# Optimization experiments

Measured on AMD Instinct MI355X. Metric: run time of the kernel, lower is better.

Reference implementation:

```python
import jax, jax.numpy as jnp
import numpy as np

D_MODEL = 1024
D_HEAD = 64
MAX_REL = 8
B, T = 4, 4096


def setup_inputs() -> dict:
    key = jax.random.key(0)
    k1, k2, k3, k4, k5 = jax.random.split(key, 5)
    return {
        "x": jax.random.normal(k1, (B, T, D_MODEL), dtype=jnp.float32),
        "W_q": jax.random.normal(k2, (D_HEAD, D_MODEL), dtype=jnp.float32) * (1.0 / np.sqrt(D_MODEL)),
        "W_k": jax.random.normal(k3, (D_HEAD, D_MODEL), dtype=jnp.float32) * (1.0 / np.sqrt(D_MODEL)),
        "W_v": jax.random.normal(k4, (D_HEAD, D_MODEL), dtype=jnp.float32) * (1.0 / np.sqrt(D_MODEL)),
        "rel_emb": jax.random.normal(k5, (2 * MAX_REL + 1, 1), dtype=jnp.float32),
    }


def reference(x, W_q, W_k, W_v, rel_emb):
    Bb, Tt, _ = x.shape
    scale = jnp.sqrt(jnp.asarray(W_q.shape[0], dtype=x.dtype))
    # projections (Linear: x @ W.T)
    q = jnp.einsum("btd,hd->bth", x, W_q)
    k = jnp.einsum("btd,hd->bth", x, W_k)
    v = jnp.einsum("btd,hd->bth", x, W_v)
    scores = jnp.einsum("bth,bsh->bts", q, k) / scale  # [B,T,T]
    # relative position bias: rel_emb[clip(j-i, -M, M) + M]
    i_idx = jnp.arange(Tt)[:, None]
    j_idx = jnp.arange(Tt)[None, :]
    rel = jnp.clip(j_idx - i_idx, -MAX_REL, MAX_REL) + MAX_REL  # [T,T] int
    rel_bias = rel_emb[rel, 0]  # [T,T]
    scores = scores + rel_bias[None, :, :]
    causal = j_idx <= i_idx  # [T,T] lower-triangular
    scores = jnp.where(causal[None, :, :], scores, -jnp.inf)
    attn = jax.nn.softmax(scores, axis=-1)
    return jnp.einsum("bts,bsh->bth", attn, v)
```

## Files before the change

kernel.cpp:

```cpp
#include <hip/hip_runtime.h>
#include <hip/hip_bf16.h>

#define BT 4
#define TT 4096
#define DM 1024
#define DH 64
#define NRE 17
#define LOG2E 1.4426950408889634f

using bf16 = __hip_bfloat16;
typedef __attribute__((ext_vector_type(8))) short short8;
typedef __attribute__((ext_vector_type(4))) short short4v;
typedef __attribute__((ext_vector_type(4))) float float4v;

static __device__ __forceinline__ short8 load8(const bf16* p) {
    return *reinterpret_cast<const short8*>(p);
}
static __device__ __forceinline__ short bfbits(float x) {
    return (short)__bfloat16_as_ushort(__float2bfloat16(x));
}
static __device__ __forceinline__ short8 pack8(float4v a, float4v b) {
    short8 r;
    r[0] = bfbits(a[0]); r[1] = bfbits(a[1]); r[2] = bfbits(a[2]); r[3] = bfbits(a[3]);
    r[4] = bfbits(b[0]); r[5] = bfbits(b[1]); r[6] = bfbits(b[2]); r[7] = bfbits(b[3]);
    return r;
}
static __device__ __forceinline__ void gload_lds16(const void* g, void* l) {
    __builtin_amdgcn_global_load_lds(
        (const __attribute__((address_space(1))) void*)g,
        (__attribute__((address_space(3))) void*)l, 16, 0, 0);
}


__global__ __launch_bounds__(256) void w_prep(
    const float* __restrict__ Wq, const float* __restrict__ Wk,
    const float* __restrict__ Wv, bf16* __restrict__ Wswz)
{
    const unsigned g = blockIdx.x * 256 + threadIdx.x;
    const unsigned c    = g / 768;
    const unsigned rem  = g - c * 768;
    const unsigned pair = rem >> 3;
    const unsigned slot = rem & 7;
    const unsigned l    = slot ^ (pair & 7);
    const unsigned row  = 2 * pair + (l >> 2);
    const unsigned k    = 32 * c + (l & 3) * 8;
    const float* src = (row < 64) ? &Wq[(size_t)row * DM + k]
                     : (row < 128) ? &Wk[(size_t)(row - 64) * DM + k]
                                   : &Wv[(size_t)(row - 128) * DM + k];
    float4v a = *reinterpret_cast<const float4v*>(src);
    float4v b = *reinterpret_cast<const float4v*>(src + 4);
    *reinterpret_cast<short8*>(&Wswz[(size_t)g * 8]) = pack8(a, b);
}

__global__ __launch_bounds__(256, 2) void qkv_gemm(
    const float* __restrict__ x, const bf16* __restrict__ Wswz,
    bf16* __restrict__ Qb, bf16* __restrict__ Kswz, bf16* __restrict__ Vswz)
{
    __shared__ float xs[2][64 * 32];
    __shared__ short Wls[2][96 * 64];
    __shared__ short Kimg[4096];
    __shared__ short Vimg[4096];

    const int w    = threadIdx.x >> 6;
    const int lane = threadIdx.x & 63;
    const int quad = lane >> 4;
    const int l16  = lane & 15;
    const int row0 = blockIdx.x * 64;
    const int b_   = row0 >> 12;
    const int tile = (row0 & (TT - 1)) >> 6;

    float4v acc[12];
#pragma unroll
    for (int i = 0; i < 12; i++) acc[i] = (float4v)(0.f);

    auto stage = [&](int c, int p) {
#pragma unroll
        for (int i = 0; i < 2; i++) {
            const int call = 2 * w + i;
            const int row  = call * 8 + (lane >> 3);
            const int ul   = (lane & 7) ^ (row & 7);
            gload_lds16(&x[(size_t)(row0 + row) * DM + c * 32 + ul * 4],
                        &xs[p][call * 256]);
        }
#pragma unroll
        for (int i = 0; i < 3; i++) {
            const int call = 3 * w + i;
            gload_lds16(&Wswz[(size_t)c * 6144 + call * 512 + lane * 8],
                        &Wls[p][call * 512]);
        }
    };

    stage(0, 0);

    for (int c = 0; c < 32; c++) {
        const int p = c & 1;
        __syncthreads();
        if (c + 1 < 32) stage(c + 1, p ^ 1);

        const int R = 16 * w + l16;
        float4v a0 = *reinterpret_cast<const float4v*>(
            &xs[p][R * 32 + 4 * ((2 * quad) ^ (l16 & 7))]);
        float4v a1 = *reinterpret_cast<const float4v*>(
            &xs[p][R * 32 + 4 * ((2 * quad + 1) ^ (l16 & 7))]);
        short8 a = pack8(a0, a1);
#pragma unroll
        for (int nt = 0; nt < 12; nt++) {
            const int pair = 8 * nt + (l16 >> 1);
            const int phys = ((l16 & 1) * 4 + quad) ^ (l16 >> 1);
            short8 bfr = *reinterpret_cast<const short8*>(&Wls[p][pair * 64 + phys * 8]);
            acc[nt] = __builtin_amdgcn_mfma_f32_16x16x32_bf16(a, bfr, acc[nt], 0, 0, 0);
        }
    }

#pragma unroll
    for (int nt = 0; nt < 12; nt++) {
#pragma unroll
        for (int r = 0; r < 4; r++) {
            const short hb = bfbits(acc[nt][r]);
            if (nt < 4) {
                const int i = row0 + 16 * w + quad * 4 + r;
                Qb[(size_t)i * DH + 16 * nt + l16] = __hip_bfloat16_raw{(unsigned short)hb};
            } else if (nt < 8) {
                const int h  = (nt - 4) >> 1;
                const int qk = ((nt - 4) & 1) * 2 + (l16 >> 3);
                Kimg[((2 * w + h) * 64 + qk * 16 + 4 * quad + r) * 8 + (l16 & 7)] = hb;
            }
        }
        if (nt >= 8) {
            const int dh = (nt - 8) >> 1;
            const int h8 = (nt - 8) & 1;
            short4v sv;
#pragma unroll
            for (int r = 0; r < 4; r++) sv[r] = bfbits(acc[nt][r]);
            *reinterpret_cast<short4v*>(
                &Vimg[((2 * w + dh) * 64 + quad * 16 + l16) * 8 + h8 * 4]) = sv;
        }
    }
    __syncthreads();
    {
        const size_t base = ((size_t)b_ * 64 + tile) * 4096;
#pragma unroll
        for (int i = 0; i < 2; i++) {
            const int u = threadIdx.x + 256 * i;
            *reinterpret_cast<short8*>(&Kswz[base + (size_t)u * 8]) =
                *reinterpret_cast<const short8*>(&Kimg[u * 8]);
            *reinterpret_cast<short8*>(&Vswz[base + (size_t)u * 8]) =
                *reinterpret_cast<const short8*>(&Vimg[u * 8]);
        }
    }
}

__global__ __launch_bounds__(256, 2) void attn(
    const bf16* __restrict__ Qb, const bf16* __restrict__ Kswz,
    const bf16* __restrict__ Vswz, const float* __restrict__ rel,
    float* __restrict__ out)
{
    __shared__ short sbuf[2][16384];

    const int w     = threadIdx.x >> 6;
    const int lane  = threadIdx.x & 63;
    const int quad  = lane >> 4;
    const int l16   = lane & 15;
    const int qh    = w & 1;
    const int strm  = w >> 1;
    const int batch = blockIdx.x & 3;
    const int u     = blockIdx.x >> 2;
    const int t     = (u < 64) ? u : (191 - u);
    const int q0    = 32 * t;

    const float SCL = 0.125f * LOG2E;
    const float relreg = (lane < NRE) ? rel[lane] * LOG2E : 0.f;
    const float rel0 = __shfl(relreg, 0, 64);

    const size_t bbase = (size_t)batch * TT;
    const int i_row = q0 + 16 * qh + l16;

    short8 bq0, bq1;
    {
        const bf16* qp = &Qb[(bbase + i_row) * DH];
        bq0 = load8(qp + quad * 8);
        bq1 = load8(qp + 32 + quad * 8);
    }

    float4v o[4];
#pragma unroll
    for (int dt = 0; dt < 4; dt++) o[dt] = (float4v)(0.f);
    float m_st = -1e30f, l_st = 0.f;

    const int J = (q0 + 32 + 63) >> 6;
    const int C = (J + 1) >> 1;

    auto stage = [&](int c1, int p) {
        const int T = 2 * c1 + (w & 1);
        if (T >= J) return;
        const bf16* g = ((w < 2) ? Kswz : Vswz) + ((size_t)(batch * 64 + T)) * 4096;
#pragma unroll
        for (int call = 0; call < 8; call++)
            gload_lds16(g + call * 512 + lane * 8, &sbuf[p][w * 4096 + call * 512]);
    };

    stage(0, 0);

    for (int c = 0; c < C; c++) {
        const int p = c & 1;
        __syncthreads();
        if (c + 1 < C) stage(c + 1, p ^ 1);

        const int T = 2 * c + strm;
        if (T < J) {
            const int js = 64 * T;
            const short* Kl = &sbuf[p][strm * 4096];
            const short* Vl = &sbuf[p][8192 + strm * 4096];

            float4v st[4];
#pragma unroll
            for (int nt = 0; nt < 4; nt++) st[nt] = (float4v)(0.f);
#pragma unroll
            for (int nt = 0; nt < 4; nt++) {
                short8 k0 = *reinterpret_cast<const short8*>(Kl + (2 * nt) * 512 + lane * 8);
                short8 k1 = *reinterpret_cast<const short8*>(Kl + (2 * nt + 1) * 512 + lane * 8);
                st[nt] = __builtin_amdgcn_mfma_f32_16x16x32_bf16(k0, bq0, st[nt], 0, 0, 0);
                st[nt] = __builtin_amdgcn_mfma_f32_16x16x32_bf16(k1, bq1, st[nt], 0, 0, 0);
            }

            float mcur = -1e30f;
            if (js + 71 <= q0 + 16 * qh) {
#pragma unroll
                for (int nt = 0; nt < 4; nt++)
#pragma unroll
                    for (int r = 0; r < 4; r++) {
                        float v = st[nt][r] * SCL + rel0;
                        st[nt][r] = v;
                        mcur = fmaxf(mcur, v);
                    }
            } else {
#pragma unroll
                for (int nt = 0; nt < 4; nt++) {
                    const int jb = js + 16 * nt + 4 * quad;
#pragma unroll
                    for (int r = 0; r < 4; r++) {
                        const int d = jb + r - i_row;
                        int idx = d + 8;
                        idx = idx < 0 ? 0 : (idx > 16 ? 16 : idx);
                        float v = st[nt][r] * SCL + __shfl(relreg, idx, 64);
                        v = (d > 0) ? -1e30f : v;
                        st[nt][r] = v;
                        mcur = fmaxf(mcur, v);
                    }
                }
            }

            mcur = fmaxf(mcur, __shfl_xor(mcur, 16, 64));
            mcur = fmaxf(mcur, __shfl_xor(mcur, 32, 64));

            const float mn = fmaxf(m_st, mcur);
            const float alpha = exp2f(m_st - mn);
            m_st = mn;

            float lsum = 0.f;
            short4v pb[4];
#pragma unroll
            for (int nt = 0; nt < 4; nt++)
#pragma unroll
                for (int r = 0; r < 4; r++) {
                    const float e = exp2f(st[nt][r] - mn);
                    lsum += e;
                    pb[nt][r] = bfbits(e);
                }
            lsum += __shfl_xor(lsum, 16, 64);
            lsum += __shfl_xor(lsum, 32, 64);
            l_st = l_st * alpha + lsum;

#pragma unroll
            for (int dt = 0; dt < 4; dt++)
#pragma unroll
                for (int r = 0; r < 4; r++) o[dt][r] *= alpha;

#pragma unroll
            for (int nt = 0; nt < 4; nt++) {
#pragma unroll
                for (int dh = 0; dh < 2; dh++) {
                    short8 vs = *reinterpret_cast<const short8*>(
                        Vl + (nt * 2 + dh) * 512 + lane * 8);
                    short4v lo, hi;
                    lo[0] = vs[0]; lo[1] = vs[1]; lo[2] = vs[2]; lo[3] = vs[3];
                    hi[0] = vs[4]; hi[1] = vs[5]; hi[2] = vs[6]; hi[3] = vs[7];
                    o[2 * dh]     = __builtin_amdgcn_mfma_f32_16x16x16bf16_1k(lo, pb[nt], o[2 * dh], 0, 0, 0);
                    o[2 * dh + 1] = __builtin_amdgcn_mfma_f32_16x16x16bf16_1k(hi, pb[nt], o[2 * dh + 1], 0, 0, 0);
                }
            }
        }
    }

    __syncthreads();
    float* Osh = (float*)&sbuf[0][0];
    float* mM  = Osh + 4 * 16 * 68;
    float* lL  = mM + 64;

    const int slot = (strm * 2 + qh) * 16 + l16;
    if (quad == 0) { mM[slot] = m_st; lL[slot] = l_st; }
#pragma unroll
    for (int dt = 0; dt < 4; dt++)
        *reinterpret_cast<float4v*>(
            &Osh[((strm * 2 + qh) * 16 + l16) * 68 + 16 * dt + 4 * quad]) = o[dt];
    __syncthreads();

    for (int idx = threadIdx.x; idx < 32 * 64; idx += 256) {
        const int row = idx >> 6;
        const int qh2 = row >> 4, lr = row & 15;
        const int c2  = idx & 63;
        const float m0 = mM[(0 * 2 + qh2) * 16 + lr];
        const float m1 = mM[(1 * 2 + qh2) * 16 + lr];
        const float M = fmaxf(m0, m1);
        const float e0 = exp2f(m0 - M), e1 = exp2f(m1 - M);
        const float L = lL[(0 * 2 + qh2) * 16 + lr] * e0 + lL[(1 * 2 + qh2) * 16 + lr] * e1;
        const float acc = Osh[((0 * 2 + qh2) * 16 + lr) * 68 + c2] * e0
                        + Osh[((1 * 2 + qh2) * 16 + lr) * 68 + c2] * e1;
        out[(bbase + q0 + row) * DH + c2] = acc / L;
    }
}

extern "C" void kernel_launch(void* const* d_in, const int* in_sizes, int n_in,
                              void* d_out, int out_size, void* d_ws, size_t ws_size,
                              hipStream_t stream)
{
    const float* x   = (const float*)d_in[0];
    const float* Wq  = (const float*)d_in[1];
    const float* Wk  = (const float*)d_in[2];
    const float* Wv  = (const float*)d_in[3];
    const float* rel = (const float*)d_in[4];
    float* out = (float*)d_out;

    bf16* Qb   = (bf16*)d_ws;
    bf16* Kswz = Qb   + (size_t)BT * TT * DH;
    bf16* Vswz = Kswz + (size_t)BT * TT * DH;
    bf16* Wswz = Vswz + (size_t)BT * TT * DH;

    w_prep<<<96, 256, 0, stream>>>(Wq, Wk, Wv, Wswz);
    qkv_gemm<<<256, 256, 0, stream>>>(x, Wswz, Qb, Kswz, Vswz);
    attn<<<512, 256, 0, stream>>>(Qb, Kswz, Vswz, rel, out);
}
```

Baseline: 170.7 us.

## Restructure QKV GEMM and attention into 32-row tiles with per-wave KV streams

The QKV GEMM now uses 32-row blocks (twice as many blocks) with a 64-wide K step, splits the output columns across waves, and reads LDS through inline ds_read_b128 with a single wait. K/V are re-laid out as 32-key tiles. Attention is reorganised so each of four waves owns its own stream of 32-key tiles, double-buffered per wave without block-wide barriers, handling both 16-row query halves, and a 4-way merge combines the partial softmax states. The block-to-query-tile mapping is also changed. The goals are more parallelism, finer causal granularity and less barrier stalling, at the cost of more merge work and more register pressure.

```diff
diff --git a/kernel.cpp b/kernel.cpp
--- a/kernel.cpp
+++ b/kernel.cpp
@@ -13,6 +13,8 @@
 typedef __attribute__((ext_vector_type(4))) short short4v;
 typedef __attribute__((ext_vector_type(4))) float float4v;
 
+#define BC8(x) __builtin_bit_cast(short8, x)
+
 static __device__ __forceinline__ short8 load8(const bf16* p) {
     return *reinterpret_cast<const short8*>(p);
 }
@@ -30,6 +32,12 @@
         (const __attribute__((address_space(1))) void*)g,
         (__attribute__((address_space(3))) void*)l, 16, 0, 0);
 }
+static __device__ __forceinline__ unsigned lds_addr(const void* p) {
+    return (unsigned)(size_t)(const __attribute__((address_space(3))) void*)p;
+}
+
+#define DSR(dst, addr, off) \
+    asm volatile("ds_read_b128 %0, %1 offset:" off : "=v"(dst) : "v"(addr))
 
 
 __global__ __launch_bounds__(256) void w_prep(
@@ -56,97 +64,123 @@
     const float* __restrict__ x, const bf16* __restrict__ Wswz,
     bf16* __restrict__ Qb, bf16* __restrict__ Kswz, bf16* __restrict__ Vswz)
 {
-    __shared__ float xs[2][64 * 32];
-    __shared__ short Wls[2][96 * 64];
-    __shared__ short Kimg[4096];
-    __shared__ short Vimg[4096];
+    __shared__ __align__(16) float xs[2][2048];
+    __shared__ __align__(16) short Wls[2][12288];
 
     const int w    = threadIdx.x >> 6;
     const int lane = threadIdx.x & 63;
     const int quad = lane >> 4;
     const int l16  = lane & 15;
-    const int row0 = blockIdx.x * 64;
-    const int b_   = row0 >> 12;
-    const int tile = (row0 & (TT - 1)) >> 6;
-
-    float4v acc[12];
-#pragma unroll
-    for (int i = 0; i < 12; i++) acc[i] = (float4v)(0.f);
+    const int half = w & 1;
+    const int colh = w >> 1;
+    const int row0 = blockIdx.x * 32;
+
+    float4v acc[6];
+#pragma unroll
+    for (int i = 0; i < 6; i++) acc[i] = (float4v)(0.f);
 
     auto stage = [&](int c, int p) {
 #pragma unroll
-        for (int i = 0; i < 2; i++) {
-            const int call = 2 * w + i;
-            const int row  = call * 8 + (lane >> 3);
-            const int ul   = (lane & 7) ^ (row & 7);
-            gload_lds16(&x[(size_t)(row0 + row) * DM + c * 32 + ul * 4],
+        for (int j = 0; j < 2; j++) {
+            const int call = 2 * w + j;
+            const int row  = 4 * call + (lane >> 4);
+            const int pu   = lane & 15;
+            const int gu   = (pu & 8) | ((pu ^ row) & 7);
+            gload_lds16(&x[(size_t)(row0 + row) * DM + c * 64 + gu * 4],
                         &xs[p][call * 256]);
         }
 #pragma unroll
-        for (int i = 0; i < 3; i++) {
-            const int call = 3 * w + i;
-            gload_lds16(&Wswz[(size_t)c * 6144 + call * 512 + lane * 8],
+        for (int j = 0; j < 6; j++) {
+            const int call = 6 * w + j;
+            gload_lds16(&Wswz[(size_t)(2 * c) * 6144 + call * 512 + lane * 8],
                         &Wls[p][call * 512]);
         }
     };
 
+    const unsigned xlds = lds_addr(&xs[0][0]);
+    const unsigned wlds = lds_addr(&Wls[0][0]);
+    const int R        = 16 * half + l16;
+    const int lo3_0    = (2 * quad)     ^ (R & 7);
+    const int lo3_1    = (2 * quad + 1) ^ (R & 7);
+    const int pairBase = 48 * colh + (l16 >> 1);
+    const int physW    = ((l16 & 1) * 4 + quad) ^ ((l16 >> 1) & 7);
+
     stage(0, 0);
 
-    for (int c = 0; c < 32; c++) {
+    for (int c = 0; c < 16; c++) {
         const int p = c & 1;
         __syncthreads();
-        if (c + 1 < 32) stage(c + 1, p ^ 1);
-
-        const int R = 16 * w + l16;
-        float4v a0 = *reinterpret_cast<const float4v*>(
-            &xs[p][R * 32 + 4 * ((2 * quad) ^ (l16 & 7))]);
-        float4v a1 = *reinterpret_cast<const float4v*>(
-            &xs[p][R * 32 + 4 * ((2 * quad + 1) ^ (l16 & 7))]);
-        short8 a = pack8(a0, a1);
-#pragma unroll
-        for (int nt = 0; nt < 12; nt++) {
-            const int pair = 8 * nt + (l16 >> 1);
-            const int phys = ((l16 & 1) * 4 + quad) ^ (l16 >> 1);
-            short8 bfr = *reinterpret_cast<const short8*>(&Wls[p][pair * 64 + phys * 8]);
-            acc[nt] = __builtin_amdgcn_mfma_f32_16x16x32_bf16(a, bfr, acc[nt], 0, 0, 0);
-        }
-    }
-
-#pragma unroll
-    for (int nt = 0; nt < 12; nt++) {
+        if (c + 1 < 16) stage(c + 1, p ^ 1);
+
+        const unsigned xb  = xlds + (unsigned)(p * 8192) + R * 64 * 4;
+        const unsigned xa0 = xb + lo3_0 * 16;
+        const unsigned xa1 = xb + lo3_1 * 16;
+        const unsigned wa  = wlds + (unsigned)(p * 24576) + pairBase * 128 + physW * 16;
+
+        float4v x00, x01, x10, x11;
+        float4v w00, w01, w02, w03, w04, w05, w10, w11, w12, w13, w14, w15;
+        DSR(x00, xa0, "0");   DSR(x10, xa0, "128");
+        DSR(x01, xa1, "0");   DSR(x11, xa1, "128");
+        DSR(w00, wa, "0");     DSR(w01, wa, "1024");  DSR(w02, wa, "2048");
+        DSR(w03, wa, "3072");  DSR(w04, wa, "4096");  DSR(w05, wa, "5120");
+        DSR(w10, wa, "12288"); DSR(w11, wa, "13312"); DSR(w12, wa, "14336");
+        DSR(w13, wa, "15360"); DSR(w14, wa, "16384"); DSR(w15, wa, "17408");
+        asm volatile("s_waitcnt lgkmcnt(0)"
+            : "+v"(x00), "+v"(x01), "+v"(x10), "+v"(x11),
+              "+v"(w00), "+v"(w01), "+v"(w02), "+v"(w03), "+v"(w04), "+v"(w05),
+              "+v"(w10), "+v"(w11), "+v"(w12), "+v"(w13), "+v"(w14), "+v"(w15));
+
+        short8 a0 = pack8(x00, x01);
+        short8 a1 = pack8(x10, x11);
+        acc[0] = __builtin_amdgcn_mfma_f32_16x16x32_bf16(a0, BC8(w00), acc[0], 0, 0, 0);
+        acc[1] = __builtin_amdgcn_mfma_f32_16x16x32_bf16(a0, BC8(w01), acc[1], 0, 0, 0);
+        acc[2] = __builtin_amdgcn_mfma_f32_16x16x32_bf16(a0, BC8(w02), acc[2], 0, 0, 0);
+        acc[3] = __builtin_amdgcn_mfma_f32_16x16x32_bf16(a0, BC8(w03), acc[3], 0, 0, 0);
+        acc[4] = __builtin_amdgcn_mfma_f32_16x16x32_bf16(a0, BC8(w04), acc[4], 0, 0, 0);
+        acc[5] = __builtin_amdgcn_mfma_f32_16x16x32_bf16(a0, BC8(w05), acc[5], 0, 0, 0);
+        acc[0] = __builtin_amdgcn_mfma_f32_16x16x32_bf16(a1, BC8(w10), acc[0], 0, 0, 0);
+        acc[1] = __builtin_amdgcn_mfma_f32_16x16x32_bf16(a1, BC8(w11), acc[1], 0, 0, 0);
+        acc[2] = __builtin_amdgcn_mfma_f32_16x16x32_bf16(a1, BC8(w12), acc[2], 0, 0, 0);
+        acc[3] = __builtin_amdgcn_mfma_f32_16x16x32_bf16(a1, BC8(w13), acc[3], 0, 0, 0);
+        acc[4] = __builtin_amdgcn_mfma_f32_16x16x32_bf16(a1, BC8(w14), acc[4], 0, 0, 0);
+        acc[5] = __builtin_amdgcn_mfma_f32_16x16x32_bf16(a1, BC8(w15), acc[5], 0, 0, 0);
+    }
+
+    __syncthreads();
+    short* Kimg = (short*)&xs[0][0];
+    short* Vimg = Kimg + 2048;
+#pragma unroll
+    for (int nt = 0; nt < 6; nt++) {
+        const int cc = 96 * colh + 16 * nt + l16;
 #pragma unroll
         for (int r = 0; r < 4; r++) {
+            const int jl = 16 * half + 4 * quad + r;
             const short hb = bfbits(acc[nt][r]);
-            if (nt < 4) {
-                const int i = row0 + 16 * w + quad * 4 + r;
-                Qb[(size_t)i * DH + 16 * nt + l16] = __hip_bfloat16_raw{(unsigned short)hb};
-            } else if (nt < 8) {
-                const int h  = (nt - 4) >> 1;
-                const int qk = ((nt - 4) & 1) * 2 + (l16 >> 3);
-                Kimg[((2 * w + h) * 64 + qk * 16 + 4 * quad + r) * 8 + (l16 & 7)] = hb;
+            if (cc < 64) {
+                Qb[(size_t)(row0 + jl) * DH + cc] = __hip_bfloat16_raw{(unsigned short)hb};
+            } else if (cc < 128) {
+                const int k  = cc - 64;
+                const int h  = k >> 5;
+                const int q2 = (k & 31) >> 3;
+                Kimg[((2 * half + h) * 64 + q2 * 16 + 4 * quad + r) * 8 + (k & 7)] = hb;
+            } else {
+                const int d  = cc - 128;
+                const int dh = d >> 5;
+                const int hi = (d >> 4) & 1;
+                Vimg[((2 * half + dh) * 64 + quad * 16 + (d & 15)) * 8 + hi * 4 + r] = hb;
             }
-        }
-        if (nt >= 8) {
-            const int dh = (nt - 8) >> 1;
-            const int h8 = (nt - 8) & 1;
-            short4v sv;
-#pragma unroll
-            for (int r = 0; r < 4; r++) sv[r] = bfbits(acc[nt][r]);
-            *reinterpret_cast<short4v*>(
-                &Vimg[((2 * w + dh) * 64 + quad * 16 + l16) * 8 + h8 * 4]) = sv;
         }
     }
     __syncthreads();
     {
-        const size_t base = ((size_t)b_ * 64 + tile) * 4096;
-#pragma unroll
-        for (int i = 0; i < 2; i++) {
-            const int u = threadIdx.x + 256 * i;
-            *reinterpret_cast<short8*>(&Kswz[base + (size_t)u * 8]) =
-                *reinterpret_cast<const short8*>(&Kimg[u * 8]);
-            *reinterpret_cast<short8*>(&Vswz[base + (size_t)u * 8]) =
-                *reinterpret_cast<const short8*>(&Vimg[u * 8]);
-        }
+        const int b_     = row0 >> 12;
+        const int tile32 = (row0 & (TT - 1)) >> 5;
+        const size_t base = ((size_t)(b_ * 512 + tile32 * 4)) * 512;
+        const int u = threadIdx.x;
+        *reinterpret_cast<short8*>(&Kswz[base + (size_t)u * 8]) =
+            *reinterpret_cast<const short8*>(&Kimg[u * 8]);
+        *reinterpret_cast<short8*>(&Vswz[base + (size_t)u * 8]) =
+            *reinterpret_cast<const short8*>(&Vimg[u * 8]);
     }
 }
 
@@ -155,96 +189,110 @@
     const bf16* __restrict__ Vswz, const float* __restrict__ rel,
     float* __restrict__ out)
 {
-    __shared__ short sbuf[2][16384];
+    __shared__ __align__(16) short sbuf[32768];
 
     const int w     = threadIdx.x >> 6;
     const int lane  = threadIdx.x & 63;
     const int quad  = lane >> 4;
     const int l16   = lane & 15;
-    const int qh    = w & 1;
-    const int strm  = w >> 1;
     const int batch = blockIdx.x & 3;
     const int u     = blockIdx.x >> 2;
-    const int t     = (u < 64) ? u : (191 - u);
+    const int t     = (u & 1) ? (127 - (u >> 1)) : (u >> 1);
     const int q0    = 32 * t;
 
     const float SCL = 0.125f * LOG2E;
-    const float relreg = (lane < NRE) ? rel[lane] * LOG2E : 0.f;
+    float relreg = 0.f;
+    if (lane < NRE) relreg = rel[lane] * LOG2E;
     const float rel0 = __shfl(relreg, 0, 64);
 
     const size_t bbase = (size_t)batch * TT;
-    const int i_row = q0 + 16 * qh + l16;
-
-    short8 bq0, bq1;
-    {
-        const bf16* qp = &Qb[(bbase + i_row) * DH];
-        bq0 = load8(qp + quad * 8);
-        bq1 = load8(qp + 32 + quad * 8);
-    }
-
-    float4v o[4];
-#pragma unroll
-    for (int dt = 0; dt < 4; dt++) o[dt] = (float4v)(0.f);
-    float m_st = -1e30f, l_st = 0.f;
-
-    const int J = (q0 + 32 + 63) >> 6;
-    const int C = (J + 1) >> 1;
-
-    auto stage = [&](int c1, int p) {
-        const int T = 2 * c1 + (w & 1);
-        if (T >= J) return;
-        const bf16* g = ((w < 2) ? Kswz : Vswz) + ((size_t)(batch * 64 + T)) * 4096;
-#pragma unroll
-        for (int call = 0; call < 8; call++)
-            gload_lds16(g + call * 512 + lane * 8, &sbuf[p][w * 4096 + call * 512]);
+
+    short8 bq[2][2];
+#pragma unroll
+    for (int qh = 0; qh < 2; qh++) {
+        const bf16* qp = &Qb[(bbase + q0 + 16 * qh + l16) * DH];
+        bq[qh][0] = load8(qp + quad * 8);
+        bq[qh][1] = load8(qp + 32 + quad * 8);
+    }
+    __builtin_amdgcn_s_waitcnt(0xF70);
+
+    float4v o[2][4];
+#pragma unroll
+    for (int qh = 0; qh < 2; qh++)
+#pragma unroll
+        for (int dt = 0; dt < 4; dt++) o[qh][dt] = (float4v)(0.f);
+    float m_st[2] = {-1e30f, -1e30f}, l_st[2] = {0.f, 0.f};
+
+    short* mybuf = &sbuf[w * 8192];
+    const unsigned sbase = lds_addr(&sbuf[0]) + (unsigned)(w * 16384 + lane * 16);
+
+    auto stageKV = [&](int T, int p) {
+        const size_t gb = ((size_t)(batch * 512 + T * 4)) * 512;
+        short* dK = mybuf + p * 4096;
+#pragma unroll
+        for (int j = 0; j < 4; j++)
+            gload_lds16(&Kswz[gb + j * 512 + lane * 8], dK + j * 512);
+#pragma unroll
+        for (int j = 0; j < 4; j++)
+            gload_lds16(&Vswz[gb + j * 512 + lane * 8], dK + 2048 + j * 512);
     };
 
-    stage(0, 0);
-
-    for (int c = 0; c < C; c++) {
-        const int p = c & 1;
-        __syncthreads();
-        if (c + 1 < C) stage(c + 1, p ^ 1);
-
-        const int T = 2 * c + strm;
-        if (T < J) {
-            const int js = 64 * T;
-            const short* Kl = &sbuf[p][strm * 4096];
-            const short* Vl = &sbuf[p][8192 + strm * 4096];
-
-            float4v st[4];
-#pragma unroll
-            for (int nt = 0; nt < 4; nt++) st[nt] = (float4v)(0.f);
-#pragma unroll
-            for (int nt = 0; nt < 4; nt++) {
-                short8 k0 = *reinterpret_cast<const short8*>(Kl + (2 * nt) * 512 + lane * 8);
-                short8 k1 = *reinterpret_cast<const short8*>(Kl + (2 * nt + 1) * 512 + lane * 8);
-                st[nt] = __builtin_amdgcn_mfma_f32_16x16x32_bf16(k0, bq0, st[nt], 0, 0, 0);
-                st[nt] = __builtin_amdgcn_mfma_f32_16x16x32_bf16(k1, bq1, st[nt], 0, 0, 0);
-            }
-
+    const int cnt = (t >= w) ? (((t - w) >> 2) + 1) : 0;
+    if (cnt > 0) stageKV(w, 0);
+
+    for (int k = 0; k < cnt; k++) {
+        const int T = w + 4 * k;
+        const int p = k & 1;
+        if (k + 1 < cnt) {
+            stageKV(w + 4 * (k + 1), p ^ 1);
+            __builtin_amdgcn_s_waitcnt(0xF78);
+        } else {
+            __builtin_amdgcn_s_waitcnt(0xF70);
+        }
+
+        const unsigned ab = sbase + (unsigned)(p * 8192);
+        float4v kf0, kf1, kf2, kf3, vf0, vf1, vf2, vf3;
+        DSR(kf0, ab, "0");    DSR(kf1, ab, "1024");
+        DSR(kf2, ab, "2048"); DSR(kf3, ab, "3072");
+        DSR(vf0, ab, "4096"); DSR(vf1, ab, "5120");
+        DSR(vf2, ab, "6144"); DSR(vf3, ab, "7168");
+        asm volatile("s_waitcnt lgkmcnt(0)"
+            : "+v"(kf0), "+v"(kf1), "+v"(kf2), "+v"(kf3),
+              "+v"(vf0), "+v"(vf1), "+v"(vf2), "+v"(vf3));
+
+        const int js = 32 * T;
+#pragma unroll
+        for (int qh = 0; qh < 2; qh++) {
+            float4v st[2];
+            st[0] = (float4v)(0.f); st[1] = (float4v)(0.f);
+            st[0] = __builtin_amdgcn_mfma_f32_16x16x32_bf16(BC8(kf0), bq[qh][0], st[0], 0, 0, 0);
+            st[0] = __builtin_amdgcn_mfma_f32_16x16x32_bf16(BC8(kf1), bq[qh][1], st[0], 0, 0, 0);
+            st[1] = __builtin_amdgcn_mfma_f32_16x16x32_bf16(BC8(kf2), bq[qh][0], st[1], 0, 0, 0);
+            st[1] = __builtin_amdgcn_mfma_f32_16x16x32_bf16(BC8(kf3), bq[qh][1], st[1], 0, 0, 0);
+
+            const int i_row = q0 + 16 * qh + l16;
             float mcur = -1e30f;
-            if (js + 71 <= q0 + 16 * qh) {
-#pragma unroll
-                for (int nt = 0; nt < 4; nt++)
+            if (js + 40 <= q0 + 16 * qh) {
+#pragma unroll
+                for (int n = 0; n < 2; n++)
 #pragma unroll
                     for (int r = 0; r < 4; r++) {
-                        float v = st[nt][r] * SCL + rel0;
-                        st[nt][r] = v;
+                        float v = st[n][r] * SCL + rel0;
+                        st[n][r] = v;
                         mcur = fmaxf(mcur, v);
                     }
             } else {
 #pragma unroll
-                for (int nt = 0; nt < 4; nt++) {
-                    const int jb = js + 16 * nt + 4 * quad;
+                for (int n = 0; n < 2; n++) {
+                    const int jb = js + 16 * n + 4 * quad;
 #pragma unroll
                     for (int r = 0; r < 4; r++) {
                         const int d = jb + r - i_row;
                         int idx = d + 8;
                         idx = idx < 0 ? 0 : (idx > 16 ? 16 : idx);
-                        float v = st[nt][r] * SCL + __shfl(relreg, idx, 64);
+                        float v = st[n][r] * SCL + __shfl(relreg, idx, 64);
                         v = (d > 0) ? -1e30f : v;
-                        st[nt][r] = v;
+                        st[n][r] = v;
                         mcur = fmaxf(mcur, v);
                     }
                 }
@@ -253,70 +301,74 @@
             mcur = fmaxf(mcur, __shfl_xor(mcur, 16, 64));
             mcur = fmaxf(mcur, __shfl_xor(mcur, 32, 64));
 
-            const float mn = fmaxf(m_st, mcur);
-            const float alpha = exp2f(m_st - mn);
-            m_st = mn;
+            const float mn = fmaxf(m_st[qh], mcur);
+            const float alpha = exp2f(m_st[qh] - mn);
+            m_st[qh] = mn;
 
             float lsum = 0.f;
-            short4v pb[4];
-#pragma unroll
-            for (int nt = 0; nt < 4; nt++)
+            short4v pb[2];
+#pragma unroll
+            for (int n = 0; n < 2; n++)
 #pragma unroll
                 for (int r = 0; r < 4; r++) {
-                    const float e = exp2f(st[nt][r] - mn);
+                    const float e = exp2f(st[n][r] - mn);
                     lsum += e;
-                    pb[nt][r] = bfbits(e);
+                    pb[n][r] = bfbits(e);
                 }
             lsum += __shfl_xor(lsum, 16, 64);
             lsum += __shfl_xor(lsum, 32, 64);
-            l_st = l_st * alpha + lsum;
+            l_st[qh] = l_st[qh] * alpha + lsum;
 
 #pragma unroll
             for (int dt = 0; dt < 4; dt++)
 #pragma unroll
-                for (int r = 0; r < 4; r++) o[dt][r] *= alpha;
-
-#pragma unroll
-            for (int nt = 0; nt < 4; nt++) {
+                for (int r = 0; r < 4; r++) o[qh][dt][r] *= alpha;
+
+#pragma unroll
+            for (int n = 0; n < 2; n++) {
 #pragma unroll
                 for (int dh = 0; dh < 2; dh++) {
-                    short8 vs = *reinterpret_cast<const short8*>(
-                        Vl + (nt * 2 + dh) * 512 + lane * 8);
+                    const short8 vs = BC8((dh == 0) ? ((n == 0) ? vf0 : vf2)
+                                                    : ((n == 0) ? vf1 : vf3));
                     short4v lo, hi;
                     lo[0] = vs[0]; lo[1] = vs[1]; lo[2] = vs[2]; lo[3] = vs[3];
                     hi[0] = vs[4]; hi[1] = vs[5]; hi[2] = vs[6]; hi[3] = vs[7];
-                    o[2 * dh]     = __builtin_amdgcn_mfma_f32_16x16x16bf16_1k(lo, pb[nt], o[2 * dh], 0, 0, 0);
-                    o[2 * dh + 1] = __builtin_amdgcn_mfma_f32_16x16x16bf16_1k(hi, pb[nt], o[2 * dh + 1], 0, 0, 0);
+                    o[qh][2 * dh]     = __builtin_amdgcn_mfma_f32_16x16x16bf16_1k(lo, pb[n], o[qh][2 * dh], 0, 0, 0);
+                    o[qh][2 * dh + 1] = __builtin_amdgcn_mfma_f32_16x16x16bf16_1k(hi, pb[n], o[qh][2 * dh + 1], 0, 0, 0);
                 }
             }
         }
     }
 
     __syncthreads();
-    float* Osh = (float*)&sbuf[0][0];
-    float* mM  = Osh + 4 * 16 * 68;
-    float* lL  = mM + 64;
-
-    const int slot = (strm * 2 + qh) * 16 + l16;
-    if (quad == 0) { mM[slot] = m_st; lL[slot] = l_st; }
-#pragma unroll
-    for (int dt = 0; dt < 4; dt++)
-        *reinterpret_cast<float4v*>(
-            &Osh[((strm * 2 + qh) * 16 + l16) * 68 + 16 * dt + 4 * quad]) = o[dt];
+    float* Osh = (float*)&sbuf[0];
+    float* mM  = Osh + 4 * 32 * 68;
+    float* lL  = mM + 128;
+
+#pragma unroll
+    for (int qh = 0; qh < 2; qh++) {
+        const int row = w * 32 + 16 * qh + l16;
+        if (quad == 0) { mM[row] = m_st[qh]; lL[row] = l_st[qh]; }
+#pragma unroll
+        for (int dt = 0; dt < 4; dt++)
+            *reinterpret_cast<float4v*>(&Osh[row * 68 + 16 * dt + 4 * quad]) = o[qh][dt];
+    }
     __syncthreads();
 
     for (int idx = threadIdx.x; idx < 32 * 64; idx += 256) {
         const int row = idx >> 6;
-        const int qh2 = row >> 4, lr = row & 15;
-        const int c2  = idx & 63;
-        const float m0 = mM[(0 * 2 + qh2) * 16 + lr];
-        const float m1 = mM[(1 * 2 + qh2) * 16 + lr];
-        const float M = fmaxf(m0, m1);
-        const float e0 = exp2f(m0 - M), e1 = exp2f(m1 - M);
-        const float L = lL[(0 * 2 + qh2) * 16 + lr] * e0 + lL[(1 * 2 + qh2) * 16 + lr] * e1;
-        const float acc = Osh[((0 * 2 + qh2) * 16 + lr) * 68 + c2] * e0
-                        + Osh[((1 * 2 + qh2) * 16 + lr) * 68 + c2] * e1;
-        out[(bbase + q0 + row) * DH + c2] = acc / L;
+        const int col = idx & 63;
+        float M = mM[row];
+#pragma unroll
+        for (int s = 1; s < 4; s++) M = fmaxf(M, mM[s * 32 + row]);
+        float L = 0.f, acc = 0.f;
+#pragma unroll
+        for (int s = 0; s < 4; s++) {
+            const float e = exp2f(mM[s * 32 + row] - M);
+            L   += lL[s * 32 + row] * e;
+            acc += Osh[(s * 32 + row) * 68 + col] * e;
+        }
+        out[(bbase + q0 + row) * DH + col] = acc / L;
     }
 }
 
@@ -337,6 +389,6 @@
     bf16* Wswz = Vswz + (size_t)BT * TT * DH;
 
     w_prep<<<96, 256, 0, stream>>>(Wq, Wk, Wv, Wswz);
-    qkv_gemm<<<256, 256, 0, stream>>>(x, Wswz, Qb, Kswz, Vswz);
+    qkv_gemm<<<512, 256, 0, stream>>>(x, Wswz, Qb, Kswz, Vswz);
     attn<<<512, 256, 0, stream>>>(Qb, Kswz, Vswz, rel, out);
 }
```

Measured after the change: 160.9 us. 1.06x faster.
